# Optimization experiments

Hardware: AMD Instinct MI355X
Metric: run time of the kernel (lower is better)

## Reference

```python
import jax, jax.numpy as jnp
import numpy as np

B, N, C, H, MLP = 4, 1024, 768, 6, 2304  # num_heads = C // 128
D = C // H  # head dim = 128


def setup_inputs() -> dict:
    key = jax.random.key(0)
    ks = iter(jax.random.split(key, 64))
    def nrm(shape, s=0.02):
        return jax.random.normal(next(ks), shape, jnp.float32) * s
    inp = {}
    for nm in ("queries", "change_emb", "imageA_emb", "imageB_emb", "pe"):
        inp[nm] = jax.random.normal(next(ks), (B, N, C), jnp.float32)
    # three Attention modules: self-attn (1), change->ABC cross (2), imageAB->change cross (3)
    for i in (1, 2, 3):
        for p in ("q", "k", "v", "o"):
            inp[f"w{p}{i}"] = nrm((C, C))       # stored [in, out]; y = x @ W + b
            inp[f"b{p}{i}"] = jnp.zeros((C,), jnp.float32)
    for i in (1, 2, 3):
        inp[f"ln{i}_w"] = jnp.ones((C,), jnp.float32)
        inp[f"ln{i}_b"] = jnp.zeros((C,), jnp.float32)
    inp["mlp_w1"] = nrm((C, MLP)); inp["mlp_b1"] = jnp.zeros((MLP,), jnp.float32)
    inp["mlp_w2"] = nrm((MLP, C)); inp["mlp_b2"] = jnp.zeros((C,), jnp.float32)
    inp["flag_a"] = nrm((C,)); inp["flag_b"] = nrm((C,)); inp["flag_c"] = nrm((C,))
    return inp


def _ln(x, w, b, eps=1e-5):
    m = jnp.mean(x, -1, keepdims=True)
    v = jnp.var(x, -1, keepdims=True)
    return (x - m) * jax.lax.rsqrt(v + eps) * w + b


def _mha(q, k, v, wq, bq, wk, bk, wv, bv, wo, bo):
    b, nq, _ = q.shape
    qh = (q @ wq + bq).reshape(b, nq, H, D)
    kh = (k @ wk + bk).reshape(b, k.shape[1], H, D)
    vh = (v @ wv + bv).reshape(b, v.shape[1], H, D)
    scores = jnp.einsum('bqhd,bkhd->bhqk', qh, kh) / np.float32(np.sqrt(D))
    attn = jax.nn.softmax(scores, axis=-1)
    out = jnp.einsum('bhqk,bkhd->bqhd', attn, vh).reshape(b, nq, H * D)
    return out @ wo + bo


def reference(queries, change_emb, imageA_emb, imageB_emb, pe,
              wq1, bq1, wk1, bk1, wv1, bv1, wo1, bo1,
              wq2, bq2, wk2, bk2, wv2, bv2, wo2, bo2,
              wq3, bq3, wk3, bk3, wv3, bv3, wo3, bo3,
              ln1_w, ln1_b, ln2_w, ln2_b, ln3_w, ln3_b,
              mlp_w1, mlp_b1, mlp_w2, mlp_b2,
              flag_a, flag_b, flag_c):
    # --- self attention on change queries (skip_first_layer_add=False) ---
    q0 = queries + change_emb
    a = _mha(q0 + pe, q0 + pe, q0, wq1, bq1, wk1, bk1, wv1, bv1, wo1, bo1)
    q1 = _ln(q0 + a, ln1_w, ln1_b)
    # --- cross attention: change -> [imageA, imageB, change] ---
    qf = q1 + pe + flag_c
    k2 = jnp.concatenate((imageA_emb + pe + flag_a,
                          imageB_emb + pe + flag_b,
                          q1 + pe + flag_c), axis=1)
    v2 = jnp.concatenate((imageA_emb, imageB_emb, q1), axis=1)
    a = _mha(qf, k2, v2, wq2, bq2, wk2, bk2, wv2, bv2, wo2, bo2)
    q2 = _ln(q1 + a, ln2_w, ln2_b)
    # --- MLP (exact GELU, as nn.GELU default) ---
    mlp_out = jax.nn.gelu(q2 @ mlp_w1 + mlp_b1, approximate=False) @ mlp_w2 + mlp_b2
    q3 = _ln(q2 + mlp_out, ln3_w, ln3_b)
    change_out = q3
    # --- cross attention: [imageA; imageB] -> [image; change], batched along dim 0 ---
    qa = imageA_emb + pe + flag_a
    qb = imageB_emb + pe + flag_b
    ka = jnp.concatenate((imageA_emb + pe + flag_a, q3 + pe + flag_c), axis=1)
    kb = jnp.concatenate((imageB_emb + pe + flag_b, q3 + pe + flag_c), axis=1)
    va = jnp.concatenate((imageA_emb, q3), axis=1)
    vb = jnp.concatenate((imageB_emb, q3), axis=1)
    q = jnp.concatenate((qa, qb), axis=0)   # [2B, N, C]
    k = jnp.concatenate((ka, kb), axis=0)   # [2B, 2N, C]
    v = jnp.concatenate((va, vb), axis=0)
    a = _mha(q, k, v, wq3, bq3, wk3, bk3, wv3, bv3, wo3, bo3)
    q = q + a
    image_A_refined, image_B_refined = jnp.split(q, 2, axis=0)
    return (image_A_refined, image_B_refined, change_out)
```

## Files before the change

### kernel.cpp

```cpp
#include <hip/hip_runtime.h>
#include <hip/hip_bf16.h>
#include <math.h>

typedef short bf16x8 __attribute__((ext_vector_type(8)));
typedef float f32x4 __attribute__((ext_vector_type(4)));
using bf16_t = __hip_bfloat16;

#define DEV static __device__ __forceinline__

DEV unsigned short f2bu(float x) {
  bf16_t h = __float2bfloat16(x);
  unsigned short u;
  __builtin_memcpy(&u, &h, 2);
  return u;
}
DEV void st4(bf16_t* p, float a, float b, float c, float d) {
  ushort4 u;
  u.x = f2bu(a); u.y = f2bu(b); u.z = f2bu(c); u.w = f2bu(d);
  *reinterpret_cast<ushort4*>(p) = u;
}

DEV void async_copy16(const bf16_t* g, bf16_t* lds) {
  __builtin_amdgcn_global_load_lds(
      (const __attribute__((address_space(1))) unsigned int*)g,
      (__attribute__((address_space(3))) unsigned int*)lds, 16, 0, 0);
}

struct WPack {
  const float* s[12];
  bf16_t* d[12];
  float scale0;
};

__global__ __launch_bounds__(256) void k_wt12(WPack pk) {
  __shared__ float tile[32][33];
  int z = blockIdx.z;
  const float* W = pk.s[z];
  bf16_t* WT = pk.d[z];
  float scale = (z == 0) ? pk.scale0 : 1.0f;
  int i0 = blockIdx.x * 32;
  int o0 = blockIdx.y * 32;
  int tx = threadIdx.x & 31, ty = threadIdx.x >> 5;
  for (int r = ty; r < 32; r += 8)
    tile[r][tx] = W[(size_t)(i0 + r) * 768 + (o0 + tx)];
  __syncthreads();
  for (int r = ty; r < 32; r += 8)
    WT[(size_t)(o0 + r) * 768 + (i0 + tx)] = __float2bfloat16(tile[tx][r] * scale);
}

__global__ __launch_bounds__(256) void k_wt(const float* __restrict__ W, bf16_t* __restrict__ WT,
                                            int in_dim, int out_dim) {
  __shared__ float tile[32][33];
  int i0 = blockIdx.x * 32;
  int o0 = blockIdx.y * 32;
  int tx = threadIdx.x & 31, ty = threadIdx.x >> 5;
  for (int r = ty; r < 32; r += 8)
    tile[r][tx] = W[(size_t)(i0 + r) * out_dim + (o0 + tx)];
  __syncthreads();
  for (int r = ty; r < 32; r += 8)
    WT[(size_t)(o0 + r) * in_dim + (i0 + tx)] = __float2bfloat16(tile[tx][r]);
}

__global__ __launch_bounds__(256) void k_bqk(const float* __restrict__ bq, const float* __restrict__ bk,
                                             float* __restrict__ out, float qa) {
  int i = blockIdx.x * 256 + threadIdx.x;
  if (i < 768) out[i] = bq[i] * qa;
  else if (i < 1536) out[i] = bk[i - 768];
}

__global__ __launch_bounds__(256) void k_prep1(const float4* __restrict__ q, const float4* __restrict__ ce,
                                               const float4* __restrict__ pe,
                                               bf16_t* __restrict__ qpe_b, bf16_t* __restrict__ q0_b, int n4) {
  int i = blockIdx.x * 256 + threadIdx.x;
  if (i >= n4) return;
  float4 a = q[i], b = ce[i], p = pe[i];
  float sx = a.x + b.x, sy = a.y + b.y, sz = a.z + b.z, sw = a.w + b.w;
  st4(q0_b + 4 * (size_t)i, sx, sy, sz, sw);
  st4(qpe_b + 4 * (size_t)i, sx + p.x, sy + p.y, sz + p.z, sw + p.w);
}

__global__ __launch_bounds__(256) void k_buildqq(const float* __restrict__ imA, const float* __restrict__ imB,
                                                 const float* __restrict__ pe, const float* __restrict__ fa,
                                                 const float* __restrict__ fb, bf16_t* __restrict__ qq) {
  int idx = blockIdx.x * 256 + threadIdx.x;
  int c4 = idx % 192; int rem = idx / 192;
  int n = rem & 1023; int bb = rem >> 10;
  int b = bb & 3, isB = bb >> 2;
  int c = c4 * 4;
  size_t tok = (size_t)(b * 1024 + n) * 768 + c;
  float4 s = *(const float4*)((isB ? imB : imA) + tok);
  float4 p = *(const float4*)(pe + tok);
  float4 f = *(const float4*)((isB ? fb : fa) + c);
  st4(qq + (size_t)rem * 768 + c, s.x + p.x + f.x, s.y + p.y + f.y, s.z + p.z + f.z, s.w + p.w + f.w);
}

__global__ __launch_bounds__(256) void k_build2b(const float* __restrict__ q1,
    const float* __restrict__ imA, const float* __restrict__ imB, const float* __restrict__ pe,
    const float* __restrict__ fa, const float* __restrict__ fb, const float* __restrict__ fc,
    bf16_t* __restrict__ k2, bf16_t* __restrict__ v2, int b0) {
  int idx = blockIdx.x * 256 + threadIdx.x;
  int c4 = idx % 192; int rem = idx / 192;
  int bi = rem / 3072; int r3 = rem - bi * 3072;
  int seg = r3 >> 10; int n = r3 & 1023;
  int b = b0 + bi;
  int c = c4 * 4;
  size_t tok = (size_t)(b * 1024 + n) * 768 + c;
  float4 p = *(const float4*)(pe + tok);
  const float* srcp; const float* flg;
  if (seg == 0)      { srcp = imA + tok; flg = fa; }
  else if (seg == 1) { srcp = imB + tok; flg = fb; }
  else               { srcp = q1 + tok; flg = fc; }
  float4 s = *(const float4*)srcp;
  float4 f = *(const float4*)(flg + c);
  size_t o = (size_t)idx * 4;
  st4(v2 + o, s.x, s.y, s.z, s.w);
  st4(k2 + o, s.x + p.x + f.x, s.y + p.y + f.y, s.z + p.z + f.z, s.w + p.w + f.w);
}

__global__ __launch_bounds__(256) void k_build3b(const bf16_t* __restrict__ cf,
    const bf16_t* __restrict__ chgb,
    const float* __restrict__ imA, const float* __restrict__ imB, const float* __restrict__ pe,
    const float* __restrict__ fa, const float* __restrict__ fb,
    bf16_t* __restrict__ k3, bf16_t* __restrict__ v3, int bb0) {
  int idx = blockIdx.x * 256 + threadIdx.x;
  int c4 = idx % 192; int rem = idx / 192;
  int bi = rem >> 11; int r2 = rem & 2047;
  int seg = r2 >> 10; int n = r2 & 1023;
  int bb = bb0 + bi;
  int b = bb & 3; int isB = bb >> 2;
  int c = c4 * 4;
  size_t tok = (size_t)(b * 1024 + n) * 768 + c;
  size_t o = (size_t)idx * 4;
  if (seg == 0) {
    const float* srcp = (isB ? imB : imA);
    const float* flg = isB ? fb : fa;
    float4 p = *(const float4*)(pe + tok);
    float4 s = *(const float4*)(srcp + tok);
    float4 f = *(const float4*)(flg + c);
    st4(v3 + o, s.x, s.y, s.z, s.w);
    st4(k3 + o, s.x + p.x + f.x, s.y + p.y + f.y, s.z + p.z + f.z, s.w + p.w + f.w);
  } else {
    *reinterpret_cast<ushort4*>(v3 + o) = *reinterpret_cast<const ushort4*>(chgb + tok);
    *reinterpret_cast<ushort4*>(k3 + o) = *reinterpret_cast<const ushort4*>(cf + tok);
  }
}

__global__ __launch_bounds__(256, 3) void k_flash(
    const bf16_t* __restrict__ Q, const bf16_t* __restrict__ K,
    const bf16_t* __restrict__ Vt, bf16_t* __restrict__ O,
    int Nk, int H, int ldq, int ldk, long qStrideB, long kStrideB, long oStrideB) {
  const int z = blockIdx.y; const int b = z / H, h = z % H;
  const bf16_t* Qb = Q + (size_t)b * qStrideB + h * 128;
  const bf16_t* Kb = K + (size_t)b * kStrideB + h * 128;
  const bf16_t* Vb = Vt + (size_t)z * 128 * (size_t)Nk;
  bf16_t* Ob = O + (size_t)b * oStrideB + h * 128;
  const int q0 = blockIdx.x * 64;
  const int tid = threadIdx.x, lane = tid & 63, w = tid >> 6;
  const int g = lane >> 4, c = lane & 15;

  __shared__ bf16_t Ks[64][136];
  __shared__ bf16_t Vs[128][72];
  __shared__ bf16_t Ps[64][72];

  bf16x8 qf[4];
#pragma unroll
  for (int kk = 0; kk < 4; kk++)
    qf[kk] = *reinterpret_cast<const bf16x8*>(
        &Qb[(size_t)(q0 + w * 16 + c) * ldq + kk * 32 + g * 8]);

  f32x4 oa[8];
  float m[4], l[4];
#pragma unroll
  for (int d = 0; d < 8; d++) { f32x4 zz = {0.f, 0.f, 0.f, 0.f}; oa[d] = zz; }
#pragma unroll
  for (int r = 0; r < 4; r++) { m[r] = -1.0e30f; l[r] = 0.f; }

  const int kr_ = tid >> 4, kc_ = (tid & 15) * 8;
  const int vr_ = tid >> 3, vc_ = (tid & 7) * 8;

  const int nt = Nk >> 6;
  for (int t = 0; t < nt; ++t) {
    const int k0 = t << 6;
#pragma unroll
    for (int p = 0; p < 4; p++)
      *reinterpret_cast<uint4*>(&Ks[p * 16 + kr_][kc_]) =
          *reinterpret_cast<const uint4*>(&Kb[(size_t)(k0 + p * 16 + kr_) * ldk + kc_]);
#pragma unroll
    for (int p = 0; p < 4; p++)
      *reinterpret_cast<uint4*>(&Vs[p * 32 + vr_][vc_]) =
          *reinterpret_cast<const uint4*>(&Vb[(size_t)(p * 32 + vr_) * Nk + k0 + vc_]);
    __syncthreads();

    f32x4 s[4];
#pragma unroll
    for (int j = 0; j < 4; j++) { f32x4 zz = {0.f, 0.f, 0.f, 0.f}; s[j] = zz; }
    __builtin_amdgcn_s_setprio(1);
#pragma unroll
    for (int kk = 0; kk < 4; kk++)
#pragma unroll
      for (int j = 0; j < 4; j++) {
        bf16x8 kf = *reinterpret_cast<const bf16x8*>(&Ks[j * 16 + c][kk * 32 + g * 8]);
        s[j] = __builtin_amdgcn_mfma_f32_16x16x32_bf16(qf[kk], kf, s[j], 0, 0, 0);
      }
    __builtin_amdgcn_s_setprio(0);

    float tl[4];
#pragma unroll
    for (int r = 0; r < 4; r++)
      tl[r] = fmaxf(fmaxf(s[0][r], s[1][r]), fmaxf(s[2][r], s[3][r]));
    float ex = fmaxf(fmaxf(tl[0] - m[0], tl[1] - m[1]), fmaxf(tl[2] - m[2], tl[3] - m[3]));
    if (__any(ex > 8.0f)) {
#pragma unroll
      for (int r = 0; r < 4; r++) {
        float tv = tl[r];
        tv = fmaxf(tv, __shfl_xor(tv, 1));
        tv = fmaxf(tv, __shfl_xor(tv, 2));
        tv = fmaxf(tv, __shfl_xor(tv, 4));
        tv = fmaxf(tv, __shfl_xor(tv, 8));
        float mn = fmaxf(m[r], tv);
        float f = exp2f(m[r] - mn);
        m[r] = mn;
        l[r] *= f;
#pragma unroll
        for (int d = 0; d < 8; d++) oa[d][r] *= f;
      }
    }
#pragma unroll
    for (int j = 0; j < 4; j++)
#pragma unroll
      for (int r = 0; r < 4; r++) {
        float p = exp2f(s[j][r] - m[r]);
        l[r] += p;
        Ps[w * 16 + g * 4 + r][j * 16 + c] = __float2bfloat16(p);
      }

    __builtin_amdgcn_s_setprio(1);
#pragma unroll
    for (int kk = 0; kk < 2; kk++) {
      bf16x8 pf = *reinterpret_cast<const bf16x8*>(&Ps[w * 16 + c][kk * 32 + g * 8]);
#pragma unroll
      for (int d = 0; d < 8; d++) {
        bf16x8 vf = *reinterpret_cast<const bf16x8*>(&Vs[d * 16 + c][kk * 32 + g * 8]);
        oa[d] = __builtin_amdgcn_mfma_f32_16x16x32_bf16(pf, vf, oa[d], 0, 0, 0);
      }
    }
    __builtin_amdgcn_s_setprio(0);
    __syncthreads();
  }

  float inv[4];
#pragma unroll
  for (int r = 0; r < 4; r++) {
    float t2 = l[r];
    t2 += __shfl_xor(t2, 1);
    t2 += __shfl_xor(t2, 2);
    t2 += __shfl_xor(t2, 4);
    t2 += __shfl_xor(t2, 8);
    inv[r] = 1.0f / t2;
  }
#pragma unroll
  for (int d = 0; d < 8; d++) {
    int col = d * 16 + c;
#pragma unroll
    for (int r = 0; r < 4; r++) {
      int row = q0 + w * 16 + g * 4 + r;
      Ob[(size_t)row * 768 + col] = __float2bfloat16(oa[d][r] * inv[r]);
    }
  }
}

__global__ __launch_bounds__(256) void k_ln(const float* __restrict__ X1, const float* __restrict__ X2,
                                            const float* __restrict__ A,
                                            const float* __restrict__ w, const float* __restrict__ bvec,
                                            float* __restrict__ outf, bf16_t* __restrict__ outb,
                                            const float* __restrict__ pe, const float* __restrict__ flag,
                                            bf16_t* __restrict__ outpf) {
  int row = blockIdx.x, tid = threadIdx.x;
  size_t base = (size_t)row * 768;
  float v0 = X1[base + tid] + A[base + tid];
  float v1 = X1[base + tid + 256] + A[base + tid + 256];
  float v2 = X1[base + tid + 512] + A[base + tid + 512];
  if (X2) {
    v0 += X2[base + tid]; v1 += X2[base + tid + 256]; v2 += X2[base + tid + 512];
  }
  float s = v0 + v1 + v2;
  for (int o = 32; o; o >>= 1) s += __shfl_xor(s, o);
  __shared__ float sm[8];
  int wv = tid >> 6, ln = tid & 63;
  if (ln == 0) sm[wv] = s;
  __syncthreads();
  s = sm[0] + sm[1] + sm[2] + sm[3];
  float mean = s * (1.0f / 768.0f);
  float d0 = v0 - mean, d1 = v1 - mean, d2 = v2 - mean;
  float ss = d0 * d0 + d1 * d1 + d2 * d2;
  for (int o = 32; o; o >>= 1) ss += __shfl_xor(ss, o);
  if (ln == 0) sm[4 + wv] = ss;
  __syncthreads();
  ss = sm[4] + sm[5] + sm[6] + sm[7];
  float rstd = rsqrtf(ss * (1.0f / 768.0f) + 1e-5f);
  float o0 = d0 * rstd * w[tid] + bvec[tid];
  float o1 = d1 * rstd * w[tid + 256] + bvec[tid + 256];
  float o2 = d2 * rstd * w[tid + 512] + bvec[tid + 512];
  outf[base + tid] = o0; outf[base + tid + 256] = o1; outf[base + tid + 512] = o2;
  if (outb) {
    outb[base + tid] = __float2bfloat16(o0);
    outb[base + tid + 256] = __float2bfloat16(o1);
    outb[base + tid + 512] = __float2bfloat16(o2);
  }
  if (outpf) {
    outpf[base + tid] = __float2bfloat16(o0 + pe[base + tid] + flag[tid]);
    outpf[base + tid + 256] = __float2bfloat16(o1 + pe[base + tid + 256] + flag[tid + 256]);
    outpf[base + tid + 512] = __float2bfloat16(o2 + pe[base + tid + 512] + flag[tid + 512]);
  }
}

struct GArgs {
  const bf16_t* X; const bf16_t* Wt; const float* bias; void* Out;
  const bf16_t* resid;
  int K, ldx, ldw, ldo, vNk, mode;
  float alpha;
};

__global__ __launch_bounds__(256, 2) void k_gemmM(GArgs a0, GArgs a1, GArgs a2,
                                                  int c0, int c01, int nx0, int nx1, int nx2) {
  GArgs a; int bx, by;
  {
    int idx = blockIdx.x;
    if (idx < c0) { a = a0; bx = idx % nx0; by = idx / nx0; }
    else if (idx < c01) { idx -= c0; a = a1; bx = idx % nx1; by = idx / nx1; }
    else { idx -= c01; a = a2; bx = idx % nx2; by = idx / nx2; }
  }
  const int brow = by * 128;
  const int bcol = bx * 128;

  __shared__ bf16_t As[128 * 32];
  __shared__ bf16_t Bs[128 * 32];

  const int tid = threadIdx.x;
  const int lane = tid & 63;
  const int wave = tid >> 6;
  const int wr = wave >> 1;
  const int wc = wave & 1;

  f32x4 acc[4][4];
#pragma unroll
  for (int i = 0; i < 4; i++)
#pragma unroll
    for (int j = 0; j < 4; j++) {
      f32x4 zz = {0.f, 0.f, 0.f, 0.f};
      acc[i][j] = zz;
    }

  const int sr = lane >> 2;
  const int sc = (lane & 3) * 8;
  const int lrow = lane & 15;
  const int kch = (lane >> 4) * 8;

  const int nK = a.K >> 5;
  for (int kk = 0; kk < nK; ++kk) {
    const int k0 = kk << 5;
#pragma unroll
    for (int q = 0; q < 2; q++) {
      const int rows = wave * 32 + q * 16;
      async_copy16(a.X + (size_t)(brow + rows + sr) * a.ldx + k0 + sc, As + rows * 32);
      async_copy16(a.Wt + (size_t)(bcol + rows + sr) * a.ldw + k0 + sc, Bs + rows * 32);
    }
    __syncthreads();

    bf16x8 afr[4], bfr[4];
#pragma unroll
    for (int i = 0; i < 4; i++)
      afr[i] = *reinterpret_cast<const bf16x8*>(&As[(wr * 64 + i * 16 + lrow) * 32 + kch]);
#pragma unroll
    for (int j = 0; j < 4; j++)
      bfr[j] = *reinterpret_cast<const bf16x8*>(&Bs[(wc * 64 + j * 16 + lrow) * 32 + kch]);
#pragma unroll
    for (int i = 0; i < 4; i++)
#pragma unroll
      for (int j = 0; j < 4; j++)
        acc[i][j] = __builtin_amdgcn_mfma_f32_16x16x32_bf16(afr[i], bfr[j], acc[i][j], 0, 0, 0);
    __syncthreads();
  }

  const int lcol = lane & 15;
  const int lrow4 = (lane >> 4) * 4;

  if (a.mode == 2) {
    const int bi = brow / a.vNk;
    const int n0 = brow - bi * a.vNk;
#pragma unroll
    for (int i = 0; i < 4; i++) {
      int rloc = n0 + wr * 64 + i * 16 + lrow4;
#pragma unroll
      for (int j = 0; j < 4; j++) {
        int col = bcol + wc * 64 + j * 16 + lcol;
        int hh = col >> 7, dd = col & 127;
        float bv = a.bias[col];
        ushort4 u;
        u.x = f2bu(acc[i][j][0] + bv);
        u.y = f2bu(acc[i][j][1] + bv);
        u.z = f2bu(acc[i][j][2] + bv);
        u.w = f2bu(acc[i][j][3] + bv);
        bf16_t* dst = reinterpret_cast<bf16_t*>(a.Out) +
                      ((size_t)(bi * 6 + hh) * 128 + dd) * (size_t)a.vNk + rloc;
        *reinterpret_cast<ushort4*>(dst) = u;
      }
    }
  } else if (a.mode == 3) {
#pragma unroll
    for (int i = 0; i < 4; i++) {
      int row0 = brow + wr * 64 + i * 16 + lrow4;
#pragma unroll
      for (int j = 0; j < 4; j++) {
        int col = bcol + wc * 64 + j * 16 + lcol;
        float bv = a.bias[col];
#pragma unroll
        for (int r = 0; r < 4; r++) {
          size_t idx = (size_t)(row0 + r) * a.ldo + col;
          float rv = __bfloat162float(a.resid[(size_t)(row0 + r) * 768 + col]);
          reinterpret_cast<float*>(a.Out)[idx] = acc[i][j][r] + bv + rv;
        }
      }
    }
  } else {
#pragma unroll
    for (int i = 0; i < 4; i++) {
      int row0 = brow + wr * 64 + i * 16 + lrow4;
#pragma unroll
      for (int j = 0; j < 4; j++) {
        int col = bcol + wc * 64 + j * 16 + lcol;
        float bv = a.bias[col];
#pragma unroll
        for (int r = 0; r < 4; r++)
          reinterpret_cast<bf16_t*>(a.Out)[(size_t)(row0 + r) * a.ldo + col] =
              __float2bfloat16((acc[i][j][r] + bv) * a.alpha);
      }
    }
  }
}

static inline void gemmM3(hipStream_t st, GArgs a0, int M0, int N0,
                          GArgs a1, int M1, int N1, GArgs a2, int M2, int N2) {
  int nx0 = N0 / 128, nx1 = N1 / 128, nx2 = N2 > 0 ? N2 / 128 : 1;
  int c0 = nx0 * (M0 / 128), c1 = nx1 * (M1 / 128), c2 = nx2 * (M2 / 128);
  k_gemmM<<<dim3(c0 + c1 + c2), 256, 0, st>>>(a0, a1, a2, c0, c0 + c1, nx0, nx1, nx2);
}

template<int OUTBF, int GELU>
__global__ __launch_bounds__(256, 2) void k_gemm(
    const bf16_t* __restrict__ X, const bf16_t* __restrict__ Wt,
    const float* __restrict__ bias, void* __restrict__ Out,
    int M, int Nout, int K, int ldx, int ldw, int ldo, float alpha) {
  const int brow = blockIdx.y * 128;
  const int bcol = blockIdx.x * 128;

  __shared__ bf16_t As[128 * 32];
  __shared__ bf16_t Bs[128 * 32];

  const int tid = threadIdx.x;
  const int lane = tid & 63;
  const int wave = tid >> 6;
  const int wr = wave >> 1;
  const int wc = wave & 1;

  f32x4 acc[4][4];
#pragma unroll
  for (int i = 0; i < 4; i++)
#pragma unroll
    for (int j = 0; j < 4; j++) {
      f32x4 zz = {0.f, 0.f, 0.f, 0.f};
      acc[i][j] = zz;
    }

  const int sr = lane >> 2;
  const int sc = (lane & 3) * 8;
  const int lrow = lane & 15;
  const int kch = (lane >> 4) * 8;

  const int nK = K >> 5;
  for (int kk = 0; kk < nK; ++kk) {
    const int k0 = kk << 5;
#pragma unroll
    for (int q = 0; q < 2; q++) {
      const int rows = wave * 32 + q * 16;
      async_copy16(X + (size_t)(brow + rows + sr) * ldx + k0 + sc, As + rows * 32);
      async_copy16(Wt + (size_t)(bcol + rows + sr) * ldw + k0 + sc, Bs + rows * 32);
    }
    __syncthreads();

    bf16x8 afr[4], bfr[4];
#pragma unroll
    for (int i = 0; i < 4; i++)
      afr[i] = *reinterpret_cast<const bf16x8*>(&As[(wr * 64 + i * 16 + lrow) * 32 + kch]);
#pragma unroll
    for (int j = 0; j < 4; j++)
      bfr[j] = *reinterpret_cast<const bf16x8*>(&Bs[(wc * 64 + j * 16 + lrow) * 32 + kch]);
#pragma unroll
    for (int i = 0; i < 4; i++)
#pragma unroll
      for (int j = 0; j < 4; j++)
        acc[i][j] = __builtin_amdgcn_mfma_f32_16x16x32_bf16(afr[i], bfr[j], acc[i][j], 0, 0, 0);
    __syncthreads();
  }

  const int lcol = lane & 15;
  const int lrow4 = (lane >> 4) * 4;

#pragma unroll
  for (int i = 0; i < 4; i++) {
    int row0 = brow + wr * 64 + i * 16 + lrow4;
#pragma unroll
    for (int j = 0; j < 4; j++) {
      int col = bcol + wc * 64 + j * 16 + lcol;
      float bv = bias ? bias[col] : 0.0f;
#pragma unroll
      for (int r = 0; r < 4; r++) {
        float v = (acc[i][j][r] + bv) * alpha;
        if (GELU) v = 0.5f * v * (1.0f + erff(v * 0.70710678118f));
        size_t idx = (size_t)(row0 + r) * ldo + col;
        if (OUTBF) reinterpret_cast<bf16_t*>(Out)[idx] = __float2bfloat16(v);
        else reinterpret_cast<float*>(Out)[idx] = v;
      }
    }
  }
}

static inline void gemm(hipStream_t st, const bf16_t* X, const bf16_t* Wt, const float* bias,
                        void* out, int outBf, int gelu, int M, int N, int K,
                        int ldx, int ldw, int ldo, float alpha = 1.0f) {
  dim3 g(N / 128, M / 128), blk(256);
  if (outBf) {
    if (gelu) k_gemm<1, 1><<<g, blk, 0, st>>>(X, Wt, bias, out, M, N, K, ldx, ldw, ldo, alpha);
    else      k_gemm<1, 0><<<g, blk, 0, st>>>(X, Wt, bias, out, M, N, K, ldx, ldw, ldo, alpha);
  } else      k_gemm<0, 0><<<g, blk, 0, st>>>(X, Wt, bias, out, M, N, K, ldx, ldw, ldo, alpha);
}

extern "C" void kernel_launch(void* const* d_in, const int* in_sizes, int n_in,
                              void* d_out, int out_size, void* d_ws, size_t ws_size,
                              hipStream_t stream) {
  (void)in_sizes; (void)n_in; (void)out_size;
  constexpr int B = 4, N = 1024, C = 768, Hh = 6, MLPD = 2304;
  constexpr size_t BNC = (size_t)B * N * C;
  constexpr size_t NC  = (size_t)N * C;
  const float scale = 0.08838834764831845f;
  const float qalpha = scale * 1.4426950408889634f;

  const float* queries = (const float*)d_in[0];
  const float* change  = (const float*)d_in[1];
  const float* imA     = (const float*)d_in[2];
  const float* imB     = (const float*)d_in[3];
  const float* pe      = (const float*)d_in[4];
  const float* bq1 = (const float*)d_in[6];  const float* bk1 = (const float*)d_in[8];
  const float* bv1 = (const float*)d_in[10]; const float* bo1 = (const float*)d_in[12];
  const float* bq2 = (const float*)d_in[14]; const float* bk2 = (const float*)d_in[16];
  const float* bv2 = (const float*)d_in[18]; const float* bo2 = (const float*)d_in[20];
  const float* bq3 = (const float*)d_in[22]; const float* bk3 = (const float*)d_in[24];
  const float* bv3 = (const float*)d_in[26]; const float* bo3 = (const float*)d_in[28];
  const float* ln1w = (const float*)d_in[29]; const float* ln1b = (const float*)d_in[30];
  const float* ln2w = (const float*)d_in[31]; const float* ln2b = (const float*)d_in[32];
  const float* ln3w = (const float*)d_in[33]; const float* ln3b = (const float*)d_in[34];
  const float* mb1 = (const float*)d_in[36]; const float* mb2 = (const float*)d_in[38];
  const float* fa = (const float*)d_in[39];
  const float* fb = (const float*)d_in[40];
  const float* fc = (const float*)d_in[41];

  char* base = (char*)d_ws;
  size_t off = 0;
  auto alloc = [&](size_t bytes) -> void* {
    void* p = base + off;
    off += (bytes + 255) & ~(size_t)255;
    return p;
  };

  bf16_t* WT[14];
  const int widx[14] = {5, 7, 9, 11, 13, 15, 17, 19, 21, 23, 25, 27, 35, 37};
  for (int i = 0; i < 12; i++) WT[i] = (bf16_t*)alloc((size_t)768 * 768 * 2);
  WT[12] = (bf16_t*)alloc((size_t)768 * 2304 * 2);
  WT[13] = (bf16_t*)alloc((size_t)2304 * 768 * 2);
  float* bqk1 = (float*)alloc(1536 * 4);
  float*  q1  = (float*)alloc(BNC * 4);
  float*  q2  = (float*)alloc(BNC * 4);
  bf16_t* q2b = (bf16_t*)alloc(BNC * 2);
  bf16_t* qq   = (bf16_t*)alloc(2 * BNC * 2);
  bf16_t* Q3h  = (bf16_t*)alloc(2 * BNC * 2);
  bf16_t* qf   = (bf16_t*)alloc(BNC * 2);
  bf16_t* cf   = (bf16_t*)alloc(BNC * 2);
  bf16_t* chgb = (bf16_t*)alloc(BNC * 2);
  const size_t arena = off;

  const size_t slack = 4u << 20;
  size_t rem = (ws_size > arena + slack) ? ws_size - arena - slack : 0;
  int g2 = 4;
  while (g2 > 1 && 2 * BNC * 2 + (size_t)g2 * 4 * (3 * NC * 2) > rem) g2 >>= 1;
  int h3 = 8;
  while (h3 > 1 && BNC * 2 + (size_t)h3 * 4 * (2 * NC * 2) > rem) h3 >>= 1;

  float* dof = (float*)d_out;
  float* chg = dof + 2 * BNC;

  WPack pk;
  for (int i = 0; i < 12; i++) { pk.s[i] = (const float*)d_in[widx[i]]; pk.d[i] = WT[i]; }
  pk.scale0 = qalpha;
  k_wt12<<<dim3(24, 24, 12), 256, 0, stream>>>(pk);
  k_wt<<<dim3(24, 72), 256, 0, stream>>>((const float*)d_in[35], WT[12], 768, 2304);
  k_wt<<<dim3(72, 24), 256, 0, stream>>>((const float*)d_in[37], WT[13], 2304, 768);
  k_bqk<<<dim3(6), 256, 0, stream>>>(bq1, bk1, bqk1, qalpha);

  off = arena;
  bf16_t* qpe_b = (bf16_t*)alloc(BNC * 2);
  bf16_t* q0_b  = (bf16_t*)alloc(BNC * 2);
  bf16_t* QKh   = (bf16_t*)alloc((size_t)B * N * 1536 * 2);
  bf16_t* vT1   = (bf16_t*)alloc(BNC * 2);
  bf16_t* attC  = (bf16_t*)alloc(BNC * 2);
  float*  a1    = dof;

  k_prep1<<<dim3((int)(BNC / 4 / 256)), 256, 0, stream>>>(
      (const float4*)queries, (const float4*)change, (const float4*)pe, qpe_b, q0_b, (int)(BNC / 4));
  k_buildqq<<<dim3((int)(2 * BNC / 4 / 256)), 256, 0, stream>>>(imA, imB, pe, fa, fb, qq);
  {
    GArgs aqk = {qpe_b, WT[0], bqk1, QKh, nullptr, C, C, C, 1536, 0, 1, 1.0f};
    GArgs av  = {q0_b,  WT[2], bv1,  vT1, nullptr, C, C, C, 0,  N, 2, 1.0f};
    GArgs aq3 = {qq,    WT[8], bq3,  Q3h, nullptr, C, C, C, C,  0, 1, qalpha};
    gemmM3(stream, aqk, B * N, 1536, av, B * N, C, aq3, 2 * B * N, C);
  }
  k_flash<<<dim3(N / 64, B * Hh), 256, 0, stream>>>(QKh, QKh + 768, vT1, attC,
                                                    N, Hh, 1536, 1536,
                                                    (long)N * 1536, (long)N * 1536, (long)NC);
  gemm(stream, attC, WT[3], bo1, a1, 0, 0, B * N, C, C, C, C, C);
  k_ln<<<dim3(B * N), 256, 0, stream>>>(queries, change, a1, ln1w, ln1b, q1, (bf16_t*)nullptr,
                                        pe, fc, qf);

  off = arena;
  bf16_t* Q2h   = (bf16_t*)alloc(BNC * 2);
  bf16_t* attC2 = (bf16_t*)alloc(BNC * 2);
  bf16_t* k2in  = (bf16_t*)alloc((size_t)g2 * 3 * NC * 2);
  bf16_t* v2in  = (bf16_t*)alloc((size_t)g2 * 3 * NC * 2);
  bf16_t* K2h   = (bf16_t*)alloc((size_t)g2 * 3 * NC * 2);
  bf16_t* vT2   = (bf16_t*)alloc((size_t)g2 * 3 * NC * 2);
  float*  a2    = dof;

  if (g2 == 4) {
    const int Nk = 3 * N;
    k_build2b<<<dim3((int)((size_t)4 * 3 * NC / 4 / 256)), 256, 0, stream>>>(
        q1, imA, imB, pe, fa, fb, fc, k2in, v2in, 0);
    GArgs aq = {qf,   WT[4], bq2, Q2h, nullptr, C, C, C, C, 0, 1, qalpha};
    GArgs ak = {k2in, WT[5], bk2, K2h, nullptr, C, C, C, C, 0, 1, 1.0f};
    GArgs av = {v2in, WT[6], bv2, vT2, nullptr, C, C, C, 0, Nk, 2, 1.0f};
    gemmM3(stream, aq, B * N, C, ak, 4 * Nk, C, av, 4 * Nk, C);
    k_flash<<<dim3(N / 64, 4 * Hh), 256, 0, stream>>>(Q2h, K2h, vT2, attC2, Nk, Hh, C, C,
                                                      (long)NC, (long)(3 * NC), (long)NC);
  } else {
    gemm(stream, qf, WT[4], bq2, Q2h, 1, 0, B * N, C, C, C, C, C, qalpha);
    for (int b0 = 0; b0 < B; b0 += g2) {
      const int Nk = 3 * N;
      k_build2b<<<dim3((int)((size_t)g2 * 3 * NC / 4 / 256)), 256, 0, stream>>>(
          q1, imA, imB, pe, fa, fb, fc, k2in, v2in, b0);
      GArgs ak = {k2in, WT[5], bk2, K2h, nullptr, C, C, C, C, 0, 1, 1.0f};
      GArgs av = {v2in, WT[6], bv2, vT2, nullptr, C, C, C, 0, Nk, 2, 1.0f};
      gemmM3(stream, ak, g2 * Nk, C, av, g2 * Nk, C, av, 0, 128);
      k_flash<<<dim3(N / 64, g2 * Hh), 256, 0, stream>>>(Q2h + (size_t)b0 * NC, K2h, vT2,
                                                         attC2 + (size_t)b0 * NC, Nk, Hh, C, C,
                                                         (long)NC, (long)(3 * NC), (long)NC);
    }
  }
  gemm(stream, attC2, WT[7], bo2, a2, 0, 0, B * N, C, C, C, C, C);
  k_ln<<<dim3(B * N), 256, 0, stream>>>(q1, (const float*)nullptr, a2, ln2w, ln2b, q2, q2b,
                                        (const float*)nullptr, (const float*)nullptr, (bf16_t*)nullptr);

  off = arena;
  bf16_t* h1 = (bf16_t*)alloc((size_t)B * N * MLPD * 2);
  float*  a3 = dof;
  gemm(stream, q2b, WT[12], mb1, h1, 1, 1, B * N, MLPD, C, C, C, MLPD);
  gemm(stream, h1, WT[13], mb2, a3, 0, 0, B * N, C, MLPD, MLPD, MLPD, C);
  k_ln<<<dim3(B * N), 256, 0, stream>>>(q2, (const float*)nullptr, a3, ln3w, ln3b, chg, chgb,
                                        pe, fc, cf);

  off = arena;
  bf16_t* attC3 = (bf16_t*)alloc(2 * BNC * 2);
  bf16_t* k3in  = (bf16_t*)alloc((size_t)h3 * 2 * NC * 2);
  bf16_t* v3in  = (bf16_t*)alloc((size_t)h3 * 2 * NC * 2);
  bf16_t* K3h   = (bf16_t*)alloc((size_t)h3 * 2 * NC * 2);
  bf16_t* vT3   = (bf16_t*)alloc((size_t)h3 * 2 * NC * 2);

  for (int bb0 = 0; bb0 < 2 * B; bb0 += h3) {
    const int Nk = 2 * N;
    k_build3b<<<dim3((int)((size_t)h3 * 2 * NC / 4 / 256)), 256, 0, stream>>>(
        cf, chgb, imA, imB, pe, fa, fb, k3in, v3in, bb0);
    GArgs ak = {k3in, WT[9],  bk3, K3h, nullptr, C, C, C, C, 0, 1, 1.0f};
    GArgs av = {v3in, WT[10], bv3, vT3, nullptr, C, C, C, 0, Nk, 2, 1.0f};
    gemmM3(stream, ak, h3 * Nk, C, av, h3 * Nk, C, av, 0, 128);
    k_flash<<<dim3(N / 64, h3 * Hh), 256, 0, stream>>>(Q3h + (size_t)bb0 * NC, K3h, vT3,
                                                       attC3 + (size_t)bb0 * NC, Nk, Hh, C, C,
                                                       (long)NC, (long)(2 * NC), (long)NC);
  }
  {
    GArgs ao = {attC3, WT[11], bo3, dof, qq, C, C, C, C, 0, 3, 1.0f};
    gemmM3(stream, ao, 2 * B * N, C, ao, 0, 128, ao, 0, 128);
  }
}
```

Before: 704.5 us.

## Deduplicate image K/V projections across attention stages and batch all GEMMs

Computes the image-token K and V projections for cross-attention 2 and 3 once per image instead of once per concatenated batch copy. It does this in a single 7-way packed GEMM launch, and drops the large concatenated k/v build buffers. The flash kernel is templated to walk up to three separately stored K/V segments per query block, so no concatenated copies are needed. This removes redundant projection FLOPs and memory traffic and drops the workspace-dependent batching loops. In exchange the kernel hardcodes N=1024 and H=6, and the arena grows because projected K/V for images is kept alive.

```diff
diff --git a/kernel.cpp b/kernel.cpp
--- a/kernel.cpp
+++ b/kernel.cpp
@@ -81,7 +81,8 @@
 
 __global__ __launch_bounds__(256) void k_buildqq(const float* __restrict__ imA, const float* __restrict__ imB,
                                                  const float* __restrict__ pe, const float* __restrict__ fa,
-                                                 const float* __restrict__ fb, bf16_t* __restrict__ qq) {
+                                                 const float* __restrict__ fb, bf16_t* __restrict__ qq,
+                                                 bf16_t* __restrict__ imAB) {
   int idx = blockIdx.x * 256 + threadIdx.x;
   int c4 = idx % 192; int rem = idx / 192;
   int n = rem & 1023; int bb = rem >> 10;
@@ -91,69 +92,24 @@
   float4 s = *(const float4*)((isB ? imB : imA) + tok);
   float4 p = *(const float4*)(pe + tok);
   float4 f = *(const float4*)((isB ? fb : fa) + c);
-  st4(qq + (size_t)rem * 768 + c, s.x + p.x + f.x, s.y + p.y + f.y, s.z + p.z + f.z, s.w + p.w + f.w);
-}
-
-__global__ __launch_bounds__(256) void k_build2b(const float* __restrict__ q1,
-    const float* __restrict__ imA, const float* __restrict__ imB, const float* __restrict__ pe,
-    const float* __restrict__ fa, const float* __restrict__ fb, const float* __restrict__ fc,
-    bf16_t* __restrict__ k2, bf16_t* __restrict__ v2, int b0) {
-  int idx = blockIdx.x * 256 + threadIdx.x;
-  int c4 = idx % 192; int rem = idx / 192;
-  int bi = rem / 3072; int r3 = rem - bi * 3072;
-  int seg = r3 >> 10; int n = r3 & 1023;
-  int b = b0 + bi;
-  int c = c4 * 4;
-  size_t tok = (size_t)(b * 1024 + n) * 768 + c;
-  float4 p = *(const float4*)(pe + tok);
-  const float* srcp; const float* flg;
-  if (seg == 0)      { srcp = imA + tok; flg = fa; }
-  else if (seg == 1) { srcp = imB + tok; flg = fb; }
-  else               { srcp = q1 + tok; flg = fc; }
-  float4 s = *(const float4*)srcp;
-  float4 f = *(const float4*)(flg + c);
-  size_t o = (size_t)idx * 4;
-  st4(v2 + o, s.x, s.y, s.z, s.w);
-  st4(k2 + o, s.x + p.x + f.x, s.y + p.y + f.y, s.z + p.z + f.z, s.w + p.w + f.w);
-}
-
-__global__ __launch_bounds__(256) void k_build3b(const bf16_t* __restrict__ cf,
-    const bf16_t* __restrict__ chgb,
-    const float* __restrict__ imA, const float* __restrict__ imB, const float* __restrict__ pe,
-    const float* __restrict__ fa, const float* __restrict__ fb,
-    bf16_t* __restrict__ k3, bf16_t* __restrict__ v3, int bb0) {
-  int idx = blockIdx.x * 256 + threadIdx.x;
-  int c4 = idx % 192; int rem = idx / 192;
-  int bi = rem >> 11; int r2 = rem & 2047;
-  int seg = r2 >> 10; int n = r2 & 1023;
-  int bb = bb0 + bi;
-  int b = bb & 3; int isB = bb >> 2;
-  int c = c4 * 4;
-  size_t tok = (size_t)(b * 1024 + n) * 768 + c;
-  size_t o = (size_t)idx * 4;
-  if (seg == 0) {
-    const float* srcp = (isB ? imB : imA);
-    const float* flg = isB ? fb : fa;
-    float4 p = *(const float4*)(pe + tok);
-    float4 s = *(const float4*)(srcp + tok);
-    float4 f = *(const float4*)(flg + c);
-    st4(v3 + o, s.x, s.y, s.z, s.w);
-    st4(k3 + o, s.x + p.x + f.x, s.y + p.y + f.y, s.z + p.z + f.z, s.w + p.w + f.w);
-  } else {
-    *reinterpret_cast<ushort4*>(v3 + o) = *reinterpret_cast<const ushort4*>(chgb + tok);
-    *reinterpret_cast<ushort4*>(k3 + o) = *reinterpret_cast<const ushort4*>(cf + tok);
-  }
-}
-
-__global__ __launch_bounds__(256, 3) void k_flash(
-    const bf16_t* __restrict__ Q, const bf16_t* __restrict__ K,
-    const bf16_t* __restrict__ Vt, bf16_t* __restrict__ O,
-    int Nk, int H, int ldq, int ldk, long qStrideB, long kStrideB, long oStrideB) {
-  const int z = blockIdx.y; const int b = z / H, h = z % H;
-  const bf16_t* Qb = Q + (size_t)b * qStrideB + h * 128;
-  const bf16_t* Kb = K + (size_t)b * kStrideB + h * 128;
-  const bf16_t* Vb = Vt + (size_t)z * 128 * (size_t)Nk;
-  bf16_t* Ob = O + (size_t)b * oStrideB + h * 128;
+  size_t o = (size_t)rem * 768 + c;
+  st4(imAB + o, s.x, s.y, s.z, s.w);
+  st4(qq + o, s.x + p.x + f.x, s.y + p.y + f.y, s.z + p.z + f.z, s.w + p.w + f.w);
+}
+
+struct FArgs {
+  const bf16_t* Q; bf16_t* O;
+  const bf16_t* Kp[3]; const bf16_t* Vp[3];
+  int badd[3], bmask[3];
+  int ldq, ldk;
+  long qStrideB, oStrideB;
+};
+
+template<int NSEG>
+__global__ __launch_bounds__(256, 3) void k_flash(FArgs fa) {
+  const int z = blockIdx.y; const int b = z / 6, h = z % 6;
+  const bf16_t* Qb = fa.Q + (size_t)b * fa.qStrideB + h * 128;
+  bf16_t* Ob = fa.O + (size_t)b * fa.oStrideB + h * 128;
   const int q0 = blockIdx.x * 64;
   const int tid = threadIdx.x, lane = tid & 63, w = tid >> 6;
   const int g = lane >> 4, c = lane & 15;
@@ -166,7 +122,7 @@
 #pragma unroll
   for (int kk = 0; kk < 4; kk++)
     qf[kk] = *reinterpret_cast<const bf16x8*>(
-        &Qb[(size_t)(q0 + w * 16 + c) * ldq + kk * 32 + g * 8]);
+        &Qb[(size_t)(q0 + w * 16 + c) * fa.ldq + kk * 32 + g * 8]);
 
   f32x4 oa[8];
   float m[4], l[4];
@@ -177,75 +133,81 @@
 
   const int kr_ = tid >> 4, kc_ = (tid & 15) * 8;
   const int vr_ = tid >> 3, vc_ = (tid & 7) * 8;
-
-  const int nt = Nk >> 6;
-  for (int t = 0; t < nt; ++t) {
-    const int k0 = t << 6;
-#pragma unroll
-    for (int p = 0; p < 4; p++)
-      *reinterpret_cast<uint4*>(&Ks[p * 16 + kr_][kc_]) =
-          *reinterpret_cast<const uint4*>(&Kb[(size_t)(k0 + p * 16 + kr_) * ldk + kc_]);
-#pragma unroll
-    for (int p = 0; p < 4; p++)
-      *reinterpret_cast<uint4*>(&Vs[p * 32 + vr_][vc_]) =
-          *reinterpret_cast<const uint4*>(&Vb[(size_t)(p * 32 + vr_) * Nk + k0 + vc_]);
-    __syncthreads();
-
-    f32x4 s[4];
-#pragma unroll
-    for (int j = 0; j < 4; j++) { f32x4 zz = {0.f, 0.f, 0.f, 0.f}; s[j] = zz; }
-    __builtin_amdgcn_s_setprio(1);
-#pragma unroll
-    for (int kk = 0; kk < 4; kk++)
-#pragma unroll
-      for (int j = 0; j < 4; j++) {
-        bf16x8 kf = *reinterpret_cast<const bf16x8*>(&Ks[j * 16 + c][kk * 32 + g * 8]);
-        s[j] = __builtin_amdgcn_mfma_f32_16x16x32_bf16(qf[kk], kf, s[j], 0, 0, 0);
+  const int ldk = fa.ldk;
+
+#pragma unroll
+  for (int s = 0; s < NSEG; ++s) {
+    const int bi = fa.badd[s] + (b & fa.bmask[s]);
+    const bf16_t* Kb = fa.Kp[s] + (size_t)bi * 1024 * ldk + h * 128;
+    const bf16_t* Vb = fa.Vp[s] + (size_t)(bi * 6 + h) * 128 * 1024;
+    for (int t = 0; t < 16; ++t) {
+      const int k0 = t << 6;
+#pragma unroll
+      for (int p = 0; p < 4; p++)
+        *reinterpret_cast<uint4*>(&Ks[p * 16 + kr_][kc_]) =
+            *reinterpret_cast<const uint4*>(&Kb[(size_t)(k0 + p * 16 + kr_) * ldk + kc_]);
+#pragma unroll
+      for (int p = 0; p < 4; p++)
+        *reinterpret_cast<uint4*>(&Vs[p * 32 + vr_][vc_]) =
+            *reinterpret_cast<const uint4*>(&Vb[(size_t)(p * 32 + vr_) * 1024 + k0 + vc_]);
+      __syncthreads();
+
+      f32x4 sx[4];
+#pragma unroll
+      for (int j = 0; j < 4; j++) { f32x4 zz = {0.f, 0.f, 0.f, 0.f}; sx[j] = zz; }
+      __builtin_amdgcn_s_setprio(1);
+#pragma unroll
+      for (int kk = 0; kk < 4; kk++)
+#pragma unroll
+        for (int j = 0; j < 4; j++) {
+          bf16x8 kf = *reinterpret_cast<const bf16x8*>(&Ks[j * 16 + c][kk * 32 + g * 8]);
+          sx[j] = __builtin_amdgcn_mfma_f32_16x16x32_bf16(qf[kk], kf, sx[j], 0, 0, 0);
+        }
+      __builtin_amdgcn_s_setprio(0);
+
+      float tl[4];
+#pragma unroll
+      for (int r = 0; r < 4; r++)
+        tl[r] = fmaxf(fmaxf(sx[0][r], sx[1][r]), fmaxf(sx[2][r], sx[3][r]));
+      float ex = fmaxf(fmaxf(tl[0] - m[0], tl[1] - m[1]), fmaxf(tl[2] - m[2], tl[3] - m[3]));
+      if (__any(ex > 8.0f)) {
+#pragma unroll
+        for (int r = 0; r < 4; r++) {
+          float tv = tl[r];
+          tv = fmaxf(tv, __shfl_xor(tv, 1));
+          tv = fmaxf(tv, __shfl_xor(tv, 2));
+          tv = fmaxf(tv, __shfl_xor(tv, 4));
+          tv = fmaxf(tv, __shfl_xor(tv, 8));
+          float mn = fmaxf(m[r], tv);
+          float f = exp2f(m[r] - mn);
+          m[r] = mn;
+          l[r] *= f;
+#pragma unroll
+          for (int d = 0; d < 8; d++) oa[d][r] *= f;
+        }
       }
-    __builtin_amdgcn_s_setprio(0);
-
-    float tl[4];
-#pragma unroll
-    for (int r = 0; r < 4; r++)
-      tl[r] = fmaxf(fmaxf(s[0][r], s[1][r]), fmaxf(s[2][r], s[3][r]));
-    float ex = fmaxf(fmaxf(tl[0] - m[0], tl[1] - m[1]), fmaxf(tl[2] - m[2], tl[3] - m[3]));
-    if (__any(ex > 8.0f)) {
-#pragma unroll
-      for (int r = 0; r < 4; r++) {
-        float tv = tl[r];
-        tv = fmaxf(tv, __shfl_xor(tv, 1));
-        tv = fmaxf(tv, __shfl_xor(tv, 2));
-        tv = fmaxf(tv, __shfl_xor(tv, 4));
-        tv = fmaxf(tv, __shfl_xor(tv, 8));
-        float mn = fmaxf(m[r], tv);
-        float f = exp2f(m[r] - mn);
-        m[r] = mn;
-        l[r] *= f;
-#pragma unroll
-        for (int d = 0; d < 8; d++) oa[d][r] *= f;
+#pragma unroll
+      for (int j = 0; j < 4; j++)
+#pragma unroll
+        for (int r = 0; r < 4; r++) {
+          float p = exp2f(sx[j][r] - m[r]);
+          l[r] += p;
+          Ps[w * 16 + g * 4 + r][j * 16 + c] = __float2bfloat16(p);
+        }
+
+      __builtin_amdgcn_s_setprio(1);
+#pragma unroll
+      for (int kk = 0; kk < 2; kk++) {
+        bf16x8 pf = *reinterpret_cast<const bf16x8*>(&Ps[w * 16 + c][kk * 32 + g * 8]);
+#pragma unroll
+        for (int d = 0; d < 8; d++) {
+          bf16x8 vf = *reinterpret_cast<const bf16x8*>(&Vs[d * 16 + c][kk * 32 + g * 8]);
+          oa[d] = __builtin_amdgcn_mfma_f32_16x16x32_bf16(pf, vf, oa[d], 0, 0, 0);
+        }
       }
-    }
-#pragma unroll
-    for (int j = 0; j < 4; j++)
-#pragma unroll
-      for (int r = 0; r < 4; r++) {
-        float p = exp2f(s[j][r] - m[r]);
-        l[r] += p;
-        Ps[w * 16 + g * 4 + r][j * 16 + c] = __float2bfloat16(p);
-      }
-
-    __builtin_amdgcn_s_setprio(1);
-#pragma unroll
-    for (int kk = 0; kk < 2; kk++) {
-      bf16x8 pf = *reinterpret_cast<const bf16x8*>(&Ps[w * 16 + c][kk * 32 + g * 8]);
-#pragma unroll
-      for (int d = 0; d < 8; d++) {
-        bf16x8 vf = *reinterpret_cast<const bf16x8*>(&Vs[d * 16 + c][kk * 32 + g * 8]);
-        oa[d] = __builtin_amdgcn_mfma_f32_16x16x32_bf16(pf, vf, oa[d], 0, 0, 0);
-      }
-    }
-    __builtin_amdgcn_s_setprio(0);
-    __syncthreads();
+      __builtin_amdgcn_s_setprio(0);
+      __syncthreads();
+    }
   }
 
   float inv[4];
@@ -320,18 +282,27 @@
   int K, ldx, ldw, ldo, vNk, mode;
   float alpha;
 };
-
-__global__ __launch_bounds__(256, 2) void k_gemmM(GArgs a0, GArgs a1, GArgs a2,
-                                                  int c0, int c01, int nx0, int nx1, int nx2) {
-  GArgs a; int bx, by;
+struct GPack {
+  GArgs a[7];
+  int cum[7];
+  int nx[7];
+};
+
+__global__ __launch_bounds__(256, 2) void k_gemmN(GPack pk) {
+  GArgs a; int base, nx;
   {
     int idx = blockIdx.x;
-    if (idx < c0) { a = a0; bx = idx % nx0; by = idx / nx0; }
-    else if (idx < c01) { idx -= c0; a = a1; bx = idx % nx1; by = idx / nx1; }
-    else { idx -= c01; a = a2; bx = idx % nx2; by = idx / nx2; }
-  }
-  const int brow = by * 128;
-  const int bcol = bx * 128;
+    if (idx < pk.cum[0])      { a = pk.a[0]; base = 0;          nx = pk.nx[0]; }
+    else if (idx < pk.cum[1]) { a = pk.a[1]; base = pk.cum[0];  nx = pk.nx[1]; }
+    else if (idx < pk.cum[2]) { a = pk.a[2]; base = pk.cum[1];  nx = pk.nx[2]; }
+    else if (idx < pk.cum[3]) { a = pk.a[3]; base = pk.cum[2];  nx = pk.nx[3]; }
+    else if (idx < pk.cum[4]) { a = pk.a[4]; base = pk.cum[3];  nx = pk.nx[4]; }
+    else if (idx < pk.cum[5]) { a = pk.a[5]; base = pk.cum[4];  nx = pk.nx[5]; }
+    else                      { a = pk.a[6]; base = pk.cum[5];  nx = pk.nx[6]; }
+  }
+  int idx = blockIdx.x - base;
+  const int brow = (idx / nx) * 128;
+  const int bcol = (idx % nx) * 128;
 
   __shared__ bf16_t As[128 * 32];
   __shared__ bf16_t Bs[128 * 32];
@@ -416,9 +387,9 @@
         float bv = a.bias[col];
 #pragma unroll
         for (int r = 0; r < 4; r++) {
-          size_t idx = (size_t)(row0 + r) * a.ldo + col;
+          size_t idx2 = (size_t)(row0 + r) * a.ldo + col;
           float rv = __bfloat162float(a.resid[(size_t)(row0 + r) * 768 + col]);
-          reinterpret_cast<float*>(a.Out)[idx] = acc[i][j][r] + bv + rv;
+          reinterpret_cast<float*>(a.Out)[idx2] = acc[i][j][r] + bv + rv;
         }
       }
     }
@@ -439,11 +410,17 @@
   }
 }
 
-static inline void gemmM3(hipStream_t st, GArgs a0, int M0, int N0,
-                          GArgs a1, int M1, int N1, GArgs a2, int M2, int N2) {
-  int nx0 = N0 / 128, nx1 = N1 / 128, nx2 = N2 > 0 ? N2 / 128 : 1;
-  int c0 = nx0 * (M0 / 128), c1 = nx1 * (M1 / 128), c2 = nx2 * (M2 / 128);
-  k_gemmM<<<dim3(c0 + c1 + c2), 256, 0, st>>>(a0, a1, a2, c0, c0 + c1, nx0, nx1, nx2);
+static inline void packN(hipStream_t st, const GArgs* as, const int* Ms, const int* Ns, int n) {
+  GPack pk;
+  int tot = 0;
+  for (int i = 0; i < 7; ++i) {
+    int j = i < n ? i : n - 1;
+    pk.a[i] = as[j];
+    pk.nx[i] = Ns[j] / 128;
+    if (i < n) tot += (Ns[j] / 128) * (Ms[j] / 128);
+    pk.cum[i] = tot;
+  }
+  k_gemmN<<<dim3(tot), 256, 0, st>>>(pk);
 }
 
 template<int OUTBF, int GELU>
@@ -538,12 +515,11 @@
 extern "C" void kernel_launch(void* const* d_in, const int* in_sizes, int n_in,
                               void* d_out, int out_size, void* d_ws, size_t ws_size,
                               hipStream_t stream) {
-  (void)in_sizes; (void)n_in; (void)out_size;
+  (void)in_sizes; (void)n_in; (void)out_size; (void)ws_size;
   constexpr int B = 4, N = 1024, C = 768, Hh = 6, MLPD = 2304;
   constexpr size_t BNC = (size_t)B * N * C;
   constexpr size_t NC  = (size_t)N * C;
-  const float scale = 0.08838834764831845f;
-  const float qalpha = scale * 1.4426950408889634f;
+  const float qalpha = 0.08838834764831845f * 1.4426950408889634f;
 
   const float* queries = (const float*)d_in[0];
   const float* change  = (const float*)d_in[1];
@@ -581,19 +557,14 @@
   float*  q1  = (float*)alloc(BNC * 4);
   float*  q2  = (float*)alloc(BNC * 4);
   bf16_t* q2b = (bf16_t*)alloc(BNC * 2);
+  bf16_t* q1b = (bf16_t*)alloc(BNC * 2);
   bf16_t* qq   = (bf16_t*)alloc(2 * BNC * 2);
   bf16_t* Q3h  = (bf16_t*)alloc(2 * BNC * 2);
-  bf16_t* qf   = (bf16_t*)alloc(BNC * 2);
-  bf16_t* cf   = (bf16_t*)alloc(BNC * 2);
-  bf16_t* chgb = (bf16_t*)alloc(BNC * 2);
+  bf16_t* K2i  = (bf16_t*)alloc(2 * BNC * 2);
+  bf16_t* vT2i = (bf16_t*)alloc(2 * BNC * 2);
+  bf16_t* K3i  = (bf16_t*)alloc(2 * BNC * 2);
+  bf16_t* vT3i = (bf16_t*)alloc(2 * BNC * 2);
   const size_t arena = off;
-
-  const size_t slack = 4u << 20;
-  size_t rem = (ws_size > arena + slack) ? ws_size - arena - slack : 0;
-  int g2 = 4;
-  while (g2 > 1 && 2 * BNC * 2 + (size_t)g2 * 4 * (3 * NC * 2) > rem) g2 >>= 1;
-  int h3 = 8;
-  while (h3 > 1 && BNC * 2 + (size_t)h3 * 4 * (2 * NC * 2) > rem) h3 >>= 1;
 
   float* dof = (float*)d_out;
   float* chg = dof + 2 * BNC;
@@ -609,6 +580,7 @@
   off = arena;
   bf16_t* qpe_b = (bf16_t*)alloc(BNC * 2);
   bf16_t* q0_b  = (bf16_t*)alloc(BNC * 2);
+  bf16_t* imAB  = (bf16_t*)alloc(2 * BNC * 2);
   bf16_t* QKh   = (bf16_t*)alloc((size_t)B * N * 1536 * 2);
   bf16_t* vT1   = (bf16_t*)alloc(BNC * 2);
   bf16_t* attC  = (bf16_t*)alloc(BNC * 2);
@@ -616,52 +588,66 @@
 
   k_prep1<<<dim3((int)(BNC / 4 / 256)), 256, 0, stream>>>(
       (const float4*)queries, (const float4*)change, (const float4*)pe, qpe_b, q0_b, (int)(BNC / 4));
-  k_buildqq<<<dim3((int)(2 * BNC / 4 / 256)), 256, 0, stream>>>(imA, imB, pe, fa, fb, qq);
-  {
-    GArgs aqk = {qpe_b, WT[0], bqk1, QKh, nullptr, C, C, C, 1536, 0, 1, 1.0f};
-    GArgs av  = {q0_b,  WT[2], bv1,  vT1, nullptr, C, C, C, 0,  N, 2, 1.0f};
-    GArgs aq3 = {qq,    WT[8], bq3,  Q3h, nullptr, C, C, C, C,  0, 1, qalpha};
-    gemmM3(stream, aqk, B * N, 1536, av, B * N, C, aq3, 2 * B * N, C);
-  }
-  k_flash<<<dim3(N / 64, B * Hh), 256, 0, stream>>>(QKh, QKh + 768, vT1, attC,
-                                                    N, Hh, 1536, 1536,
-                                                    (long)N * 1536, (long)N * 1536, (long)NC);
+  k_buildqq<<<dim3((int)(2 * BNC / 4 / 256)), 256, 0, stream>>>(imA, imB, pe, fa, fb, qq, imAB);
+  {
+    GArgs as[7] = {
+      {qpe_b, WT[0], bqk1, QKh,  nullptr, C, C, C, 1536, 0,    1, 1.0f},
+      {q0_b,  WT[2], bv1,  vT1,  nullptr, C, C, C, 0,    1024, 2, 1.0f},
+      {qq,    WT[8], bq3,  Q3h,  nullptr, C, C, C, C,    0,    1, qalpha},
+      {qq,    WT[5], bk2,  K2i,  nullptr, C, C, C, C,    0,    1, 1.0f},
+      {imAB,  WT[6], bv2,  vT2i, nullptr, C, C, C, 0,    1024, 2, 1.0f},
+      {qq,    WT[9], bk3,  K3i,  nullptr, C, C, C, C,    0,    1, 1.0f},
+      {imAB,  WT[10],bv3,  vT3i, nullptr, C, C, C, 0,    1024, 2, 1.0f},
+    };
+    int Ms[7] = {B * N, B * N, 2 * B * N, 2 * B * N, 2 * B * N, 2 * B * N, 2 * B * N};
+    int Ns[7] = {1536, C, C, C, C, C, C};
+    packN(stream, as, Ms, Ns, 7);
+  }
+  {
+    FArgs f1 = {QKh, attC, {QKh + 768, QKh + 768, QKh + 768}, {vT1, vT1, vT1},
+                {0, 0, 0}, {7, 7, 7}, 1536, 1536, (long)N * 1536, (long)NC};
+    k_flash<1><<<dim3(16, B * Hh), 256, 0, stream>>>(f1);
+  }
   gemm(stream, attC, WT[3], bo1, a1, 0, 0, B * N, C, C, C, C, C);
-  k_ln<<<dim3(B * N), 256, 0, stream>>>(queries, change, a1, ln1w, ln1b, q1, (bf16_t*)nullptr,
-                                        pe, fc, qf);
+  k_ln<<<dim3(B * N), 256, 0, stream>>>(queries, change, a1, ln1w, ln1b, q1, q1b, pe, fc, nullptr);
 
   off = arena;
+  bf16_t* qf    = (bf16_t*)alloc(BNC * 2);
   bf16_t* Q2h   = (bf16_t*)alloc(BNC * 2);
+  bf16_t* K2c   = (bf16_t*)alloc(BNC * 2);
+  bf16_t* vT2c  = (bf16_t*)alloc(BNC * 2);
   bf16_t* attC2 = (bf16_t*)alloc(BNC * 2);
-  bf16_t* k2in  = (bf16_t*)alloc((size_t)g2 * 3 * NC * 2);
-  bf16_t* v2in  = (bf16_t*)alloc((size_t)g2 * 3 * NC * 2);
-  bf16_t* K2h   = (bf16_t*)alloc((size_t)g2 * 3 * NC * 2);
-  bf16_t* vT2   = (bf16_t*)alloc((size_t)g2 * 3 * NC * 2);
   float*  a2    = dof;
 
-  if (g2 == 4) {
-    const int Nk = 3 * N;
-    k_build2b<<<dim3((int)((size_t)4 * 3 * NC / 4 / 256)), 256, 0, stream>>>(
-        q1, imA, imB, pe, fa, fb, fc, k2in, v2in, 0);
-    GArgs aq = {qf,   WT[4], bq2, Q2h, nullptr, C, C, C, C, 0, 1, qalpha};
-    GArgs ak = {k2in, WT[5], bk2, K2h, nullptr, C, C, C, C, 0, 1, 1.0f};
-    GArgs av = {v2in, WT[6], bv2, vT2, nullptr, C, C, C, 0, Nk, 2, 1.0f};
-    gemmM3(stream, aq, B * N, C, ak, 4 * Nk, C, av, 4 * Nk, C);
-    k_flash<<<dim3(N / 64, 4 * Hh), 256, 0, stream>>>(Q2h, K2h, vT2, attC2, Nk, Hh, C, C,
-                                                      (long)NC, (long)(3 * NC), (long)NC);
-  } else {
-    gemm(stream, qf, WT[4], bq2, Q2h, 1, 0, B * N, C, C, C, C, C, qalpha);
-    for (int b0 = 0; b0 < B; b0 += g2) {
-      const int Nk = 3 * N;
-      k_build2b<<<dim3((int)((size_t)g2 * 3 * NC / 4 / 256)), 256, 0, stream>>>(
-          q1, imA, imB, pe, fa, fb, fc, k2in, v2in, b0);
-      GArgs ak = {k2in, WT[5], bk2, K2h, nullptr, C, C, C, C, 0, 1, 1.0f};
-      GArgs av = {v2in, WT[6], bv2, vT2, nullptr, C, C, C, 0, Nk, 2, 1.0f};
-      gemmM3(stream, ak, g2 * Nk, C, av, g2 * Nk, C, av, 0, 128);
-      k_flash<<<dim3(N / 64, g2 * Hh), 256, 0, stream>>>(Q2h + (size_t)b0 * NC, K2h, vT2,
-                                                         attC2 + (size_t)b0 * NC, Nk, Hh, C, C,
-                                                         (long)NC, (long)(3 * NC), (long)NC);
-    }
+  {
+    struct L {
+      static __global__ void run(const float* q1_, const float* pe_, const float* fc_,
+                                 bf16_t* qf_) {
+        int idx = blockIdx.x * 256 + threadIdx.x;
+        int c = (idx % 192) * 4;
+        size_t tok = (size_t)idx * 4;
+        float4 xv = *(const float4*)(q1_ + tok);
+        float4 p = *(const float4*)(pe_ + tok);
+        float4 f = *(const float4*)(fc_ + c);
+        st4(qf_ + tok, xv.x + p.x + f.x, xv.y + p.y + f.y, xv.z + p.z + f.z, xv.w + p.w + f.w);
+      }
+    };
+    L::run<<<dim3((int)(BNC / 4 / 256)), 256, 0, stream>>>(q1, pe, fc, qf);
+  }
+  {
+    GArgs as[3] = {
+      {qf,  WT[4], bq2, Q2h,  nullptr, C, C, C, C, 0,    1, qalpha},
+      {qf,  WT[5], bk2, K2c,  nullptr, C, C, C, C, 0,    1, 1.0f},
+      {q1b, WT[6], bv2, vT2c, nullptr, C, C, C, 0, 1024, 2, 1.0f},
+    };
+    int Ms[3] = {B * N, B * N, B * N};
+    int Ns[3] = {C, C, C};
+    packN(stream, as, Ms, Ns, 3);
+  }
+  {
+    FArgs f2 = {Q2h, attC2, {K2i, K2i, K2c}, {vT2i, vT2i, vT2c},
+                {0, 4, 0}, {3, 3, 3}, C, C, (long)NC, (long)NC};
+    k_flash<3><<<dim3(16, B * Hh), 256, 0, stream>>>(f2);
   }
   gemm(stream, attC2, WT[7], bo2, a2, 0, 0, B * N, C, C, C, C, C);
   k_ln<<<dim3(B * N), 256, 0, stream>>>(q1, (const float*)nullptr, a2, ln2w, ln2b, q2, q2b,
@@ -672,29 +658,34 @@
   float*  a3 = dof;
   gemm(stream, q2b, WT[12], mb1, h1, 1, 1, B * N, MLPD, C, C, C, MLPD);
   gemm(stream, h1, WT[13], mb2, a3, 0, 0, B * N, C, MLPD, MLPD, MLPD, C);
+
+  off = arena;
+  bf16_t* cf    = (bf16_t*)alloc(BNC * 2);
+  bf16_t* chgb  = (bf16_t*)alloc(BNC * 2);
+  bf16_t* K3c   = (bf16_t*)alloc(BNC * 2);
+  bf16_t* vT3c  = (bf16_t*)alloc(BNC * 2);
+  bf16_t* attC3 = (bf16_t*)alloc(2 * BNC * 2);
+
   k_ln<<<dim3(B * N), 256, 0, stream>>>(q2, (const float*)nullptr, a3, ln3w, ln3b, chg, chgb,
                                         pe, fc, cf);
-
-  off = arena;
-  bf16_t* attC3 = (bf16_t*)alloc(2 * BNC * 2);
-  bf16_t* k3in  = (bf16_t*)alloc((size_t)h3 * 2 * NC * 2);
-  bf16_t* v3in  = (bf16_t*)alloc((size_t)h3 * 2 * NC * 2);
-  bf16_t* K3h   = (bf16_t*)alloc((size_t)h3 * 2 * NC * 2);
-  bf16_t* vT3   = (bf16_t*)alloc((size_t)h3 * 2 * NC * 2);
-
-  for (int bb0 = 0; bb0 < 2 * B; bb0 += h3) {
-    const int Nk = 2 * N;
-    k_build3b<<<dim3((int)((size_t)h3 * 2 * NC / 4 / 256)), 256, 0, stream>>>(
-        cf, chgb, imA, imB, pe, fa, fb, k3in, v3in, bb0);
-    GArgs ak = {k3in, WT[9],  bk3, K3h, nullptr, C, C, C, C, 0, 1, 1.0f};
-    GArgs av = {v3in, WT[10], bv3, vT3, nullptr, C, C, C, 0, Nk, 2, 1.0f};
-    gemmM3(stream, ak, h3 * Nk, C, av, h3 * Nk, C, av, 0, 128);
-    k_flash<<<dim3(N / 64, h3 * Hh), 256, 0, stream>>>(Q3h + (size_t)bb0 * NC, K3h, vT3,
-                                                       attC3 + (size_t)bb0 * NC, Nk, Hh, C, C,
-                                                       (long)NC, (long)(2 * NC), (long)NC);
-  }
-  {
-    GArgs ao = {attC3, WT[11], bo3, dof, qq, C, C, C, C, 0, 3, 1.0f};
-    gemmM3(stream, ao, 2 * B * N, C, ao, 0, 128, ao, 0, 128);
-  }
-}
+  {
+    GArgs as[2] = {
+      {cf,   WT[9],  bk3, K3c,  nullptr, C, C, C, C, 0,    1, 1.0f},
+      {chgb, WT[10], bv3, vT3c, nullptr, C, C, C, 0, 1024, 2, 1.0f},
+    };
+    int Ms[2] = {B * N, B * N};
+    int Ns[2] = {C, C};
+    packN(stream, as, Ms, Ns, 2);
+  }
+  {
+    FArgs f3 = {Q3h, attC3, {K3i, K3c, K3c}, {vT3i, vT3c, vT3c},
+                {0, 0, 0}, {7, 3, 3}, C, C, (long)NC, (long)NC};
+    k_flash<2><<<dim3(16, 2 * B * Hh), 256, 0, stream>>>(f3);
+  }
+  {
+    GArgs as[1] = {{attC3, WT[11], bo3, dof, qq, C, C, C, C, 0, 3, 1.0f}};
+    int Ms[1] = {2 * B * N};
+    int Ns[1] = {C};
+    packN(stream, as, Ms, Ns, 1);
+  }
+}
```

Result: faster. 642.3 us (-8.8%).
